# Performance work log

Hardware: AMD Instinct MI355X
Metric: run time of the kernel (lower is better)

Reference implementation:

```python
import jax, jax.numpy as jnp
import numpy as np

K = 1024
H = 16
HID = 4 * K
EPS = 1e-5


def _layernorm(x, g, b):
    mu = jnp.mean(x, axis=-1, keepdims=True)
    var = jnp.var(x, axis=-1, keepdims=True)
    return (x - mu) * jax.lax.rsqrt(var + EPS) * g + b


def _attention(xq, xkv, wq, wk, wv, wo, bo, causal):
    b, t, e = xq.shape
    tc = xkv.shape[1]
    h, s = H, e // H
    scale = e ** (-0.25)  # applied to both q and k, as in the original
    q = (xq @ wq).reshape(b, t, h, s) * scale
    k = (xkv @ wk).reshape(b, tc, h, s) * scale
    v = (xkv @ wv).reshape(b, tc, h, s)
    dot = jnp.einsum('bqhs,bkhs->bhqk', q, k)  # (b,h,t,tc)
    if causal:
        mask = jnp.tril(jnp.ones((t, tc), dtype=bool))
        dot = jnp.where(mask, dot, jnp.finfo(dot.dtype).min)
    att = jax.nn.softmax(dot, axis=-1)
    out = jnp.einsum('bhqk,bkhs->bqhs', att, v).reshape(b, t, e)
    return out @ wo + bo


def setup_inputs() -> dict:
    key = jax.random.key(0)
    ks = jax.random.split(key, 16)
    sd = K ** -0.5
    inp = {
        'x': jax.random.normal(ks[0], (4, 1024, K), jnp.float32),
        'context': jax.random.normal(ks[1], (4, 1024, K), jnp.float32),
        'sa_wq': jax.random.normal(ks[2], (K, K), jnp.float32) * sd,
        'sa_wk': jax.random.normal(ks[3], (K, K), jnp.float32) * sd,
        'sa_wv': jax.random.normal(ks[4], (K, K), jnp.float32) * sd,
        'sa_wo': jax.random.normal(ks[5], (K, K), jnp.float32) * sd,
        'sa_bo': jnp.zeros((K,), jnp.float32),
        'ca_wq': jax.random.normal(ks[6], (K, K), jnp.float32) * sd,
        'ca_wk': jax.random.normal(ks[7], (K, K), jnp.float32) * sd,
        'ca_wv': jax.random.normal(ks[8], (K, K), jnp.float32) * sd,
        'ca_wo': jax.random.normal(ks[9], (K, K), jnp.float32) * sd,
        'ca_bo': jnp.zeros((K,), jnp.float32),
        'n1_g': jnp.ones((K,), jnp.float32), 'n1_b': jnp.zeros((K,), jnp.float32),
        'n2_g': jnp.ones((K,), jnp.float32), 'n2_b': jnp.zeros((K,), jnp.float32),
        'n3_g': jnp.ones((K,), jnp.float32), 'n3_b': jnp.zeros((K,), jnp.float32),
        'ff_w1': jax.random.normal(ks[10], (K, HID), jnp.float32) * sd,
        'ff_b1': jnp.zeros((HID,), jnp.float32),
        'ff_w2': jax.random.normal(ks[11], (HID, K), jnp.float32) * (HID ** -0.5),
        'ff_b2': jnp.zeros((K,), jnp.float32),
    }
    return inp


def reference(x, context, sa_wq, sa_wk, sa_wv, sa_wo, sa_bo,
              ca_wq, ca_wk, ca_wv, ca_wo, ca_bo,
              n1_g, n1_b, n2_g, n2_b, n3_g, n3_b,
              ff_w1, ff_b1, ff_w2, ff_b2):
    # Masked self-attention + residual + LN (dropout is identity in eval mode)
    sa = _attention(x, x, sa_wq, sa_wk, sa_wv, sa_wo, sa_bo, causal=True)
    x = _layernorm(x + sa, n1_g, n1_b)
    # Cross-attention + residual + LN
    ca = _attention(x, context, ca_wq, ca_wk, ca_wv, ca_wo, ca_bo, causal=False)
    x = _layernorm(x + ca, n2_g, n2_b)
    # FFN + residual + LN
    ff = jax.nn.relu(x @ ff_w1 + ff_b1) @ ff_w2 + ff_b2
    x = _layernorm(x + ff, n3_g, n3_b)
    return x
```

## Files before the change

kernel.cpp:

```cpp
#include <hip/hip_runtime.h>

typedef __bf16 bf16x8 __attribute__((ext_vector_type(8)));
typedef __bf16 bf16x4 __attribute__((ext_vector_type(4)));
typedef float floatx4 __attribute__((ext_vector_type(4)));

#define EMB 1024
#define MROWS 4096
#define HIDN 4096
#define PSTRIDE ((size_t)MROWS * EMB)

__device__ __forceinline__ void load_lds16(const __bf16* g, __bf16* l) {
    __builtin_amdgcn_global_load_lds(
        (const __attribute__((address_space(1))) void*)g,
        (__attribute__((address_space(3))) void*)l, 16, 0, 0);
}

struct TJobs { const float* s[16]; __bf16* d[16]; int sld[16]; int dld[16]; };
__global__ void transpose_cast16_kernel(TJobs a) {
    __shared__ float tile[32][33];
    int jz = blockIdx.z;
    const float* in = a.s[jz];
    __bf16* out = a.d[jz];
    int sld = a.sld[jz], dld = a.dld[jz];
    int tx = threadIdx.x, ty = threadIdx.y;
    int c0 = blockIdx.x * 32, r0 = blockIdx.y * 32;
#pragma unroll
    for (int i = 0; i < 32; i += 8)
        tile[ty + i][tx] = in[(size_t)(r0 + ty + i) * sld + c0 + tx];
    __syncthreads();
#pragma unroll
    for (int i = 0; i < 32; i += 8)
        out[(size_t)(c0 + ty + i) * dld + r0 + tx] = (__bf16)tile[tx][ty + i];
}

__global__ void transpose_v_kernel(const __bf16* __restrict__ in,
                                   __bf16* __restrict__ vt, int ld, int Tc) {
    __shared__ __bf16 tile[32][33];
    int tx = threadIdx.x, ty = threadIdx.y;
    int t0 = blockIdx.x * 32, s0 = blockIdx.y * 32;
    int bh = blockIdx.z, b = bh >> 4, h = bh & 15;
#pragma unroll
    for (int i = 0; i < 32; i += 8)
        tile[ty + i][tx] = in[(size_t)(b * Tc + t0 + ty + i) * ld + h * 64 + s0 + tx];
    __syncthreads();
#pragma unroll
    for (int i = 0; i < 32; i += 8)
        vt[((size_t)bh * 64 + s0 + ty + i) * Tc + t0 + tx] = tile[tx][ty + i];
}

__global__ void cast_bf16_kernel(const float* __restrict__ in,
                                 __bf16* __restrict__ out, int n) {
    int i = (blockIdx.x * 256 + threadIdx.x) * 4;
    if (i >= n) return;
    float4 v = *(const float4*)(in + i);
    bf16x4 o;
    o[0] = (__bf16)v.x; o[1] = (__bf16)v.y; o[2] = (__bf16)v.z; o[3] = (__bf16)v.w;
    *(bf16x4*)(out + i) = o;
}

template <int RELU, int REG>
__launch_bounds__(256, 4)
__global__ void gemm_bt(const __bf16* __restrict__ A, const __bf16* __restrict__ A2,
                        int asplit, const __bf16* __restrict__ Bt,
                        __bf16* __restrict__ cb, __bf16* __restrict__ cbalt,
                        const float* __restrict__ bias,
                        int M, int N, int Kd, float scale0, float scale1,
                        int split, int fx, int fy) {
    __shared__ alignas(16) __bf16 smem[2 * 128 * 32];
    __bf16* As = smem;
    __bf16* Bs = smem + 128 * 32;
    int tid  = threadIdx.x;
    int wv   = tid >> 6, lane = tid & 63;

    int L   = blockIdx.x + gridDim.x * (blockIdx.y + gridDim.y * blockIdx.z);
    int xcd = L & 7, j = L >> 3;
    int ff  = fx * fy;
    int zw  = xcd / ff;
    int rr  = xcd % ff;
    int nxf = gridDim.x / fx;
    int bnw = (j % nxf) * fx + (rr % fx);
    int bmw = (j / nxf) * fy + (rr / fx);
    int bn  = bnw * 128, bm = bmw * 128;

    int wm   = (wv & 1) * 64, wn = (wv >> 1) * 64;
    int l16  = lane & 15, g16 = lane >> 4;

    int kc   = Kd / gridDim.z;
    int zoff = zw * kc;

    const __bf16* Ause = (bn >= asplit) ? A2 : A;

    const __bf16* ag0 = Ause + (size_t)(bm + (tid >> 2)) * Kd + zoff + (tid & 3) * 8;
    const __bf16* ag1 = ag0 + (size_t)64 * Kd;
    const __bf16* bg0 = Bt + (size_t)(bn + (tid >> 2)) * Kd + zoff + (tid & 3) * 8;
    const __bf16* bg1 = bg0 + (size_t)64 * Kd;
    __bf16* al0 = &As[tid * 8];
    __bf16* al1 = &As[2048 + tid * 8];
    __bf16* bl0 = &Bs[tid * 8];
    __bf16* bl1 = &Bs[2048 + tid * 8];

    floatx4 acc[4][4] = {};

    if (REG) {
        bf16x8 pa0 = *(const bf16x8*)ag0;
        bf16x8 pa1 = *(const bf16x8*)ag1;
        bf16x8 pb0 = *(const bf16x8*)bg0;
        bf16x8 pb1 = *(const bf16x8*)bg1;
        for (int k0 = 0; k0 < kc; k0 += 32) {
            *(bf16x8*)al0 = pa0;
            *(bf16x8*)al1 = pa1;
            *(bf16x8*)bl0 = pb0;
            *(bf16x8*)bl1 = pb1;
            if (k0 + 32 < kc) {
                ag0 += 32; ag1 += 32; bg0 += 32; bg1 += 32;
                pa0 = *(const bf16x8*)ag0;
                pa1 = *(const bf16x8*)ag1;
                pb0 = *(const bf16x8*)bg0;
                pb1 = *(const bf16x8*)bg1;
            }
            __syncthreads();
            bf16x8 af[4], bfr[4];
#pragma unroll
            for (int i = 0; i < 4; ++i)
                af[i] = *(const bf16x8*)&As[(wm + i * 16 + l16) * 32 + g16 * 8];
#pragma unroll
            for (int jj = 0; jj < 4; ++jj)
                bfr[jj] = *(const bf16x8*)&Bs[(wn + jj * 16 + l16) * 32 + g16 * 8];
#pragma unroll
            for (int i = 0; i < 4; ++i)
#pragma unroll
                for (int jj = 0; jj < 4; ++jj)
                    acc[i][jj] = __builtin_amdgcn_mfma_f32_16x16x32_bf16(af[i], bfr[jj], acc[i][jj], 0, 0, 0);
            __syncthreads();
        }
    } else {
        for (int k0 = 0; k0 < kc; k0 += 32) {
            __syncthreads();
            load_lds16(ag0, al0); load_lds16(ag1, al1);
            load_lds16(bg0, bl0); load_lds16(bg1, bl1);
            ag0 += 32; ag1 += 32; bg0 += 32; bg1 += 32;
            __syncthreads();
            bf16x8 af[4], bfr[4];
#pragma unroll
            for (int i = 0; i < 4; ++i)
                af[i] = *(const bf16x8*)&As[(wm + i * 16 + l16) * 32 + g16 * 8];
#pragma unroll
            for (int jj = 0; jj < 4; ++jj)
                bfr[jj] = *(const bf16x8*)&Bs[(wn + jj * 16 + l16) * 32 + g16 * 8];
#pragma unroll
            for (int i = 0; i < 4; ++i)
#pragma unroll
                for (int jj = 0; jj < 4; ++jj)
                    acc[i][jj] = __builtin_amdgcn_mfma_f32_16x16x32_bf16(af[i], bfr[jj], acc[i][jj], 0, 0, 0);
        }
        __syncthreads();
    }

    __bf16* Cp = (zw == 0) ? cb : cbalt + (size_t)(zw - 1) * M * N;
    const float* bz = (zw == 0) ? bias : nullptr;

    __bf16* eb = smem + wv * 2048;
    int erow = lane >> 2;
    int ecol = (lane & 3) * 16;
#pragma unroll
    for (int i = 0; i < 4; ++i) {
#pragma unroll
        for (int jj = 0; jj < 4; ++jj) {
            int col  = bn + wn + jj * 16 + l16;
            float sc = (col < split) ? scale0 : scale1;
            float bv = bz ? bz[col] : 0.f;
#pragma unroll
            for (int r = 0; r < 4; ++r) {
                float v = acc[i][jj][r] * sc + bv;
                if (RELU) v = fmaxf(v, 0.f);
                eb[(g16 * 4 + r) * 76 + jj * 16 + l16] = (__bf16)v;
            }
        }
        bf16x8 t0 = *(const bf16x8*)&eb[erow * 76 + ecol];
        bf16x8 t1 = *(const bf16x8*)&eb[erow * 76 + ecol + 8];
        size_t gb = (size_t)(bm + wm + i * 16 + erow) * N + bn + wn + ecol;
        *(bf16x8*)&Cp[gb]     = t0;
        *(bf16x8*)&Cp[gb + 8] = t1;
    }
}


#define VM4 asm volatile("s_waitcnt vmcnt(4)" ::: "memory")
#define VM0 asm volatile("s_waitcnt vmcnt(0)" ::: "memory")

#define STG(GB, HROWS, LDST, TILE)                                             \
    do {                                                                       \
        load_lds16((GB) + (size_t)(HROWS) * Kd + (TILE) * 64, (LDST) + tid8);  \
        load_lds16((GB) + (size_t)((HROWS) + 128) * Kd + (TILE) * 64,          \
                   (LDST) + 4096 + tid8);                                      \
    } while (0)

#define RD_A(ABUF, QM)                                                         \
    _Pragma("unroll")                                                          \
    for (int i2 = 0; i2 < 4; ++i2) {                                           \
        int s_ = (QM) * 128 + wr64 + i2 * 16 + l16;                            \
        a_[i2][0] = *(const bf16x8*)&(ABUF)[s_ * 64 + pa0];                    \
        a_[i2][1] = *(const bf16x8*)&(ABUF)[s_ * 64 + pa1];                    \
    }

#define RD_B(BBUF, QN, BREG)                                                   \
    _Pragma("unroll")                                                          \
    for (int j2 = 0; j2 < 2; ++j2) {                                           \
        int s_ = (QN) * 128 + wc32 + j2 * 16 + l16;                            \
        BREG[j2][0] = *(const bf16x8*)&(BBUF)[s_ * 64 + pa0];                  \
        BREG[j2][1] = *(const bf16x8*)&(BBUF)[s_ * 64 + pa1];                  \
    }

#define CORE(QM, QN, BREG, STAGE, TAIL)                                         \
    {                                                                           \
        STAGE;                                                                  \
        __builtin_amdgcn_s_setprio(1);                                          \
        _Pragma("unroll")                                                       \
        for (int i2 = 0; i2 < 4; ++i2)                                          \
            _Pragma("unroll")                                                   \
            for (int j2 = 0; j2 < 2; ++j2) {                                    \
                acc[(QM) * 4 + i2][(QN) * 2 + j2] =                             \
                    __builtin_amdgcn_mfma_f32_16x16x32_bf16(                    \
                        a_[i2][0], BREG[j2][0],                                 \
                        acc[(QM) * 4 + i2][(QN) * 2 + j2], 0, 0, 0);            \
                acc[(QM) * 4 + i2][(QN) * 2 + j2] =                             \
                    __builtin_amdgcn_mfma_f32_16x16x32_bf16(                    \
                        a_[i2][1], BREG[j2][1],                                 \
                        acc[(QM) * 4 + i2][(QN) * 2 + j2], 0, 0, 0);            \
            }                                                                   \
        __builtin_amdgcn_s_setprio(0);                                          \
        TAIL;                                                                   \
        __builtin_amdgcn_s_barrier();                                           \
    }

template <int RELU>
__launch_bounds__(512, 2)
__global__ void gemm256(const __bf16* __restrict__ A, const __bf16* __restrict__ A2,
                        int asplit, const __bf16* __restrict__ Bt,
                        __bf16* __restrict__ C, __bf16* __restrict__ Calt,
                        const float* __restrict__ bias,
                        int M, int N, int Kd, float scale0, float scale1,
                        int split, int pw) {
    __shared__ alignas(16) __bf16 smem[65536];
    __bf16* Alds0 = smem;
    __bf16* Alds1 = smem + 16384;
    __bf16* Blds0 = smem + 32768;
    __bf16* Blds1 = smem + 49152;

    int tid = threadIdx.x;
    int wv = tid >> 6, lane = tid & 63;
    int l16 = lane & 15, g16 = lane >> 4;
    int wr = wv >> 2, wc = wv & 3;
    int wr64 = wr * 64, wc32 = wc * 32;
    int pa0 = (g16 ^ (l16 & 7)) * 8;
    int pa1 = pa0 ^ 32;

    int L = blockIdx.x;
    int xcd = L & 7, jj = L >> 3;
    int bm = ((xcd >> 1) * 4 + jj / pw) * 256;
    int bn = ((xcd & 1) * pw + jj % pw) * 256;

    int z = blockIdx.y;
    int kc = Kd / gridDim.y;
    int zoff = z * kc;

    const __bf16* Ause = (bn >= asplit) ? A2 : A;
    int tid8 = tid * 8;
    int colOff = ((tid & 7) ^ ((tid >> 3) & 7)) * 8;
    const __bf16* baseA = Ause + (size_t)(bm + (tid >> 3)) * Kd + zoff + colOff;
    const __bf16* baseB = Bt + (size_t)(bn + (tid >> 8) * 64 + ((tid >> 3) & 31)) * Kd + zoff + colOff;

    floatx4 acc[8][4] = {};
    bf16x8 a_[4][2], b0_[2][2], b1_[2][2];

    STG(baseA, 0,  Alds0,        0);
    STG(baseB, 0,  Blds0,        0);
    STG(baseA, 64, Alds0 + 8192, 0);
    STG(baseB, 32, Blds0 + 8192, 0);
    STG(baseA, 0,  Alds1,        1);
    STG(baseB, 0,  Blds1,        1);
    VM4;
    __builtin_amdgcn_s_barrier();

    int niter = kc >> 7;
    for (int t = 0; t < niter - 1; ++t) {
        int tv = 2 * t + 1, tn0 = 2 * t + 2, tn1 = 2 * t + 3;
        RD_B(Blds0, 0, b0_); RD_A(Alds0, 0);
        CORE(0, 0, b0_, STG(baseA, 64, Alds1 + 8192, tv),  (void)0);
        RD_B(Blds0, 1, b1_);
        CORE(0, 1, b1_, STG(baseB, 32, Blds1 + 8192, tv),  (void)0);
        RD_A(Alds0, 1);
        CORE(1, 0, b0_, STG(baseA, 0,  Alds0,        tn0), (void)0);
        CORE(1, 1, b1_, STG(baseB, 0,  Blds0,        tn0), VM4);
        RD_B(Blds1, 0, b0_); RD_A(Alds1, 0);
        CORE(0, 0, b0_, STG(baseA, 64, Alds0 + 8192, tn0), (void)0);
        RD_B(Blds1, 1, b1_);
        CORE(0, 1, b1_, STG(baseB, 32, Blds0 + 8192, tn0), (void)0);
        RD_A(Alds1, 1);
        CORE(1, 0, b0_, STG(baseA, 0,  Alds1,        tn1), (void)0);
        CORE(1, 1, b1_, STG(baseB, 0,  Blds1,        tn1), VM4);
    }
    {
        int tv = (kc >> 6) - 1;
        RD_B(Blds0, 0, b0_); RD_A(Alds0, 0);
        CORE(0, 0, b0_, STG(baseA, 64, Alds1 + 8192, tv), (void)0);
        RD_B(Blds0, 1, b1_);
        CORE(0, 1, b1_, STG(baseB, 32, Blds1 + 8192, tv), (void)0);
        RD_A(Alds0, 1);
        CORE(1, 0, b0_, (void)0, (void)0);
        CORE(1, 1, b1_, (void)0, VM0);
        RD_B(Blds1, 0, b0_); RD_A(Alds1, 0);
        CORE(0, 0, b0_, (void)0, (void)0);
        RD_B(Blds1, 1, b1_);
        CORE(0, 1, b1_, (void)0, (void)0);
        RD_A(Alds1, 1);
        CORE(1, 0, b0_, (void)0, (void)0);
        CORE(1, 1, b1_, (void)0, (void)0);
    }

    __syncthreads();

    __bf16* Cp = (z == 0) ? C : Calt + (size_t)(z - 1) * M * N;
    const float* bz = (z == 0) ? bias : nullptr;

    __bf16* eb = smem + wv * 1216;
    int erow = lane >> 2;
    int ecol = (lane & 3) * 16;
    float sc[4], bv[4];
#pragma unroll
    for (int j = 0; j < 4; ++j) {
        int col = bn + wc * 64 + j * 16 + l16;
        sc[j] = (col < split) ? scale0 : scale1;
        bv[j] = bz ? bz[col] : 0.f;
    }
#pragma unroll
    for (int i = 0; i < 8; ++i) {
#pragma unroll
        for (int j = 0; j < 4; ++j) {
#pragma unroll
            for (int r = 0; r < 4; ++r) {
                float v = acc[i][j][r] * sc[j] + bv[j];
                if (RELU) v = fmaxf(v, 0.f);
                eb[(g16 * 4 + r) * 76 + j * 16 + l16] = (__bf16)v;
            }
        }
        bf16x8 t0 = *(const bf16x8*)&eb[erow * 76 + ecol];
        bf16x8 t1 = *(const bf16x8*)&eb[erow * 76 + ecol + 8];
        size_t gb = (size_t)(bm + wr * 128 + i * 16 + erow) * N + bn + wc * 64 + ecol;
        *(bf16x8*)&Cp[gb]     = t0;
        *(bf16x8*)&Cp[gb + 8] = t1;
    }
}

__launch_bounds__(256, 3)
__global__ void attn_kernel(const __bf16* __restrict__ qb, const __bf16* __restrict__ kb,
                            const __bf16* __restrict__ vt, int ldq, int ldk,
                            __bf16* __restrict__ out, int causal, int Tc) {
    constexpr int T = 1024;
    __shared__ alignas(16) __bf16 Qs[128 * 72];
    __shared__ alignas(16) __bf16 Ks[64 * 72];
    __shared__ alignas(16) __bf16 Vs[64 * 72];
    __shared__ alignas(16) __bf16 Ps[4][16 * 72];

    int tid = threadIdx.x;
    int wv = tid >> 6, lane = tid & 63;
    int l16 = lane & 15, g16 = lane >> 4;

    int L = blockIdx.x;
    int xcd = L & 7, idx = L >> 3;
    int i3 = idx & 7;
    int qt2 = (idx & 32) ? (7 - i3) : i3;
    int pair = xcd + 8 * (idx >> 3);
    int h = pair & 15, b = pair >> 4;

    int r0 = tid >> 3, s8 = (tid & 7) * 8;
    int r1 = r0 + 32;

#pragma unroll
    for (int p = 0; p < 4; ++p) {
        int row = r0 + p * 32;
        bf16x8 qv = *(const bf16x8*)(qb + (size_t)(b * T + qt2 * 128 + row) * ldq + h * 64 + s8);
        *(bf16x8*)&Qs[row * 72 + s8] = qv;
    }

    floatx4 oacc[2][4] = {};
    float li[2] = {0.f, 0.f};

    int ktend = causal ? (2 * qt2 + 2) : (Tc / 64);

    const __bf16* kbase = kb + (size_t)b * Tc * ldk + h * 64 + s8;
    const __bf16* vbase = vt + (size_t)(b * 16 + h) * 64 * Tc + s8;

    bf16x8 kc0 = *(const bf16x8*)(kbase + (size_t)r0 * ldk);
    bf16x8 kc1 = *(const bf16x8*)(kbase + (size_t)r1 * ldk);
    bf16x8 vc0 = *(const bf16x8*)(vbase + (size_t)r0 * Tc);
    bf16x8 vc1 = *(const bf16x8*)(vbase + (size_t)r1 * Tc);
    bf16x8 kn0, kn1, vn0, vn1;

    for (int kt = 0; kt < ktend; ++kt) {
        __syncthreads();
        *(bf16x8*)&Ks[r0 * 72 + s8] = kc0;
        *(bf16x8*)&Ks[r1 * 72 + s8] = kc1;
        *(bf16x8*)&Vs[r0 * 72 + s8] = vc0;
        *(bf16x8*)&Vs[r1 * 72 + s8] = vc1;
        if (kt + 1 < ktend) {
            const __bf16* kp = kbase + (size_t)(kt + 1) * 64 * ldk;
            const __bf16* vp = vbase + (size_t)(kt + 1) * 64;
            kn0 = *(const bf16x8*)(kp + (size_t)r0 * ldk);
            kn1 = *(const bf16x8*)(kp + (size_t)r1 * ldk);
            vn0 = *(const bf16x8*)(vp + (size_t)r0 * Tc);
            vn1 = *(const bf16x8*)(vp + (size_t)r1 * Tc);
        }
        __syncthreads();

#pragma unroll
        for (int sub = 0; sub < 2; ++sub) {
            if (causal && kt > 2 * qt2 + sub) continue;

            floatx4 sacc[4] = {};
#pragma unroll
            for (int kk = 0; kk < 2; ++kk) {
                bf16x8 bq = *(const bf16x8*)&Qs[(sub * 64 + wv * 16 + l16) * 72 + kk * 32 + g16 * 8];
#pragma unroll
                for (int j = 0; j < 4; ++j) {
                    bf16x8 ak = *(const bf16x8*)&Ks[(j * 16 + l16) * 72 + kk * 32 + g16 * 8];
                    sacc[j] = __builtin_amdgcn_mfma_f32_16x16x32_bf16(ak, bq, sacc[j], 0, 0, 0);
                }
            }
            if (causal && kt == 2 * qt2 + sub) {
                int qloc = wv * 16 + l16;
#pragma unroll
                for (int j = 0; j < 4; ++j)
#pragma unroll
                    for (int r = 0; r < 4; ++r)
                        if (j * 16 + g16 * 4 + r > qloc) sacc[j][r] = -1e30f;
            }

#pragma unroll
            for (int j = 0; j < 4; ++j) {
                bf16x4 pk;
#pragma unroll
                for (int r = 0; r < 4; ++r) {
                    float p = __builtin_amdgcn_exp2f(sacc[j][r]);
                    li[sub] += p;
                    pk[r] = (__bf16)p;
                }
                *(bf16x4*)&Ps[wv][l16 * 72 + j * 16 + g16 * 4] = pk;
            }
#pragma unroll
            for (int kk = 0; kk < 2; ++kk) {
                bf16x8 bp = *(const bf16x8*)&Ps[wv][l16 * 72 + kk * 32 + g16 * 8];
#pragma unroll
                for (int j = 0; j < 4; ++j) {
                    bf16x8 av = *(const bf16x8*)&Vs[(j * 16 + l16) * 72 + kk * 32 + g16 * 8];
                    oacc[sub][j] = __builtin_amdgcn_mfma_f32_16x16x32_bf16(av, bp, oacc[sub][j], 0, 0, 0);
                }
            }
        }
        kc0 = kn0; kc1 = kn1; vc0 = vn0; vc1 = vn1;
    }

    li[0] += __shfl_xor(li[0], 16); li[0] += __shfl_xor(li[0], 32);
    li[1] += __shfl_xor(li[1], 16); li[1] += __shfl_xor(li[1], 32);

    __syncthreads();
    int rw = lane >> 2, c4 = (lane & 3) * 16;
#pragma unroll
    for (int sub = 0; sub < 2; ++sub) {
        float inv = 1.f / li[sub];
#pragma unroll
        for (int j = 0; j < 4; ++j) {
            bf16x4 ok;
#pragma unroll
            for (int r = 0; r < 4; ++r) ok[r] = (__bf16)(oacc[sub][j][r] * inv);
            *(bf16x4*)&Ks[(wv * 16 + l16) * 72 + j * 16 + g16 * 4] = ok;
        }
        bf16x8 o0 = *(const bf16x8*)&Ks[(wv * 16 + rw) * 72 + c4];
        bf16x8 o1 = *(const bf16x8*)&Ks[(wv * 16 + rw) * 72 + c4 + 8];
        size_t ob = (size_t)(b * T + qt2 * 128 + sub * 64 + wv * 16 + rw) * EMB + h * 64 + c4;
        *(bf16x8*)&out[ob]     = o0;
        *(bf16x8*)&out[ob + 8] = o1;
    }
}

__launch_bounds__(256)
__global__ void ln_kernel(const float* __restrict__ res,
                          const __bf16* __restrict__ pb, int np,
                          const float* __restrict__ g, const float* __restrict__ be,
                          float* __restrict__ outf, __bf16* __restrict__ outb) {
    __shared__ float red[8];
    int row = blockIdx.x, tid = threadIdx.x;
    size_t base = (size_t)row * EMB;
    float4 v = ((const float4*)(res + base))[tid];
    for (int i = 0; i < np; ++i) {
        bf16x4 u = *(const bf16x4*)(pb + i * PSTRIDE + base + tid * 4);
        v.x += (float)u[0]; v.y += (float)u[1];
        v.z += (float)u[2]; v.w += (float)u[3];
    }
    float s  = v.x + v.y + v.z + v.w;
    float ss = v.x * v.x + v.y * v.y + v.z * v.z + v.w * v.w;
#pragma unroll
    for (int o = 1; o < 64; o <<= 1) { s += __shfl_xor(s, o); ss += __shfl_xor(ss, o); }
    if ((tid & 63) == 0) { red[(tid >> 6) * 2] = s; red[(tid >> 6) * 2 + 1] = ss; }
    __syncthreads();
    s  = red[0] + red[2] + red[4] + red[6];
    ss = red[1] + red[3] + red[5] + red[7];
    float mu  = s * (1.0f / 1024.0f);
    float var = ss * (1.0f / 1024.0f) - mu * mu;
    float rs  = rsqrtf(var + 1e-5f);
    float4 gg = ((const float4*)g)[tid];
    float4 bb = ((const float4*)be)[tid];
    float4 y;
    y.x = (v.x - mu) * rs * gg.x + bb.x;
    y.y = (v.y - mu) * rs * gg.y + bb.y;
    y.z = (v.z - mu) * rs * gg.z + bb.z;
    y.w = (v.w - mu) * rs * gg.w + bb.w;
    ((float4*)(outf + base))[tid] = y;
    if (outb) {
        bf16x4 o;
        o[0] = (__bf16)y.x; o[1] = (__bf16)y.y; o[2] = (__bf16)y.z; o[3] = (__bf16)y.w;
        *(bf16x4*)(outb + base + tid * 4) = o;
    }
}

extern "C" void kernel_launch(void* const* d_in, const int* in_sizes, int n_in,
                              void* d_out, int out_size, void* d_ws, size_t ws_size,
                              hipStream_t stream) {
    const float* x     = (const float*)d_in[0];
    const float* ctx   = (const float*)d_in[1];
    const float* sa_wq = (const float*)d_in[2];
    const float* sa_wk = (const float*)d_in[3];
    const float* sa_wv = (const float*)d_in[4];
    const float* sa_wo = (const float*)d_in[5];
    const float* sa_bo = (const float*)d_in[6];
    const float* ca_wq = (const float*)d_in[7];
    const float* ca_wk = (const float*)d_in[8];
    const float* ca_wv = (const float*)d_in[9];
    const float* ca_wo = (const float*)d_in[10];
    const float* ca_bo = (const float*)d_in[11];
    const float* n1_g = (const float*)d_in[12];
    const float* n1_b = (const float*)d_in[13];
    const float* n2_g = (const float*)d_in[14];
    const float* n2_b = (const float*)d_in[15];
    const float* n3_g = (const float*)d_in[16];
    const float* n3_b = (const float*)d_in[17];
    const float* ff_w1 = (const float*)d_in[18];
    const float* ff_b1 = (const float*)d_in[19];
    const float* ff_w2 = (const float*)d_in[20];
    const float* ff_b2 = (const float*)d_in[21];

    size_t off = 0;
    auto alloc = [&](size_t bytes) {
        void* p = (char*)d_ws + off;
        off += (bytes + 255) & ~(size_t)255;
        return p;
    };
    __bf16* w_sa_qkvT = (__bf16*)alloc((size_t)3 * EMB * EMB * 2);
    __bf16* w_sa_oT   = (__bf16*)alloc((size_t)EMB * EMB * 2);
    __bf16* w_ca_kvqT = (__bf16*)alloc((size_t)3 * EMB * EMB * 2);
    __bf16* w_ca_oT   = (__bf16*)alloc((size_t)EMB * EMB * 2);
    __bf16* w1T       = (__bf16*)alloc((size_t)HIDN * EMB * 2);
    __bf16* w2T       = (__bf16*)alloc((size_t)EMB * HIDN * 2);
    __bf16* xb        = (__bf16*)alloc((size_t)MROWS * EMB * 2);
    __bf16* qkv       = (__bf16*)alloc((size_t)MROWS * 3 * EMB * 2);
    __bf16* ao        = (__bf16*)alloc((size_t)MROWS * EMB * 2);
    __bf16* hid       = (__bf16*)alloc((size_t)MROWS * HIDN * 2);
    __bf16* x1b       = (__bf16*)alloc((size_t)MROWS * EMB * 2);
    __bf16* vt        = (__bf16*)alloc((size_t)MROWS * EMB * 2);
    float* res1       = (float*)alloc((size_t)MROWS * EMB * 4);
    float* res2       = (float*)alloc((size_t)MROWS * EMB * 4);

    __bf16* qkvc = qkv;
    __bf16* pbo  = qkv;
    __bf16* pbf  = xb;

    const float QSC = 0.04508422002778011f;
    const int   BIG = 1 << 30;
    dim3 tb(32, 8);

    TJobs tj;
    tj.s[0] = sa_wq; tj.d[0] = w_sa_qkvT;                          tj.sld[0] = EMB;  tj.dld[0] = EMB;
    tj.s[1] = sa_wk; tj.d[1] = w_sa_qkvT + (size_t)EMB * EMB;      tj.sld[1] = EMB;  tj.dld[1] = EMB;
    tj.s[2] = sa_wv; tj.d[2] = w_sa_qkvT + (size_t)2 * EMB * EMB;  tj.sld[2] = EMB;  tj.dld[2] = EMB;
    tj.s[3] = sa_wo; tj.d[3] = w_sa_oT;                            tj.sld[3] = EMB;  tj.dld[3] = EMB;
    tj.s[4] = ca_wk; tj.d[4] = w_ca_kvqT;                          tj.sld[4] = EMB;  tj.dld[4] = EMB;
    tj.s[5] = ca_wv; tj.d[5] = w_ca_kvqT + (size_t)EMB * EMB;      tj.sld[5] = EMB;  tj.dld[5] = EMB;
    tj.s[6] = ca_wq; tj.d[6] = w_ca_kvqT + (size_t)2 * EMB * EMB;  tj.sld[6] = EMB;  tj.dld[6] = EMB;
    tj.s[7] = ca_wo; tj.d[7] = w_ca_oT;                            tj.sld[7] = EMB;  tj.dld[7] = EMB;
    for (int c = 0; c < 4; ++c) {
        tj.s[8 + c] = ff_w1 + (size_t)c * 1024;
        tj.d[8 + c] = w1T + (size_t)c * 1024 * 1024;
        tj.sld[8 + c] = HIDN; tj.dld[8 + c] = EMB;
    }
    for (int c = 0; c < 4; ++c) {
        tj.s[12 + c] = ff_w2 + (size_t)c * 1024 * 1024;
        tj.d[12 + c] = w2T + (size_t)c * 1024;
        tj.sld[12 + c] = EMB; tj.dld[12 + c] = HIDN;
    }
    transpose_cast16_kernel<<<dim3(32, 32, 16), tb, 0, stream>>>(tj);

    cast_bf16_kernel<<<4096, 256, 0, stream>>>(x, xb, MROWS * EMB);
    gemm256<0><<<192, 512, 0, stream>>>(xb, xb, BIG, w_sa_qkvT,
        qkv, nullptr, nullptr, MROWS, 3 * EMB, EMB, QSC, 1.f, 1024, 6);
    transpose_v_kernel<<<dim3(32, 2, 64), tb, 0, stream>>>(qkv + 2 * EMB, vt, 3 * EMB, 1024);
    attn_kernel<<<512, 256, 0, stream>>>(qkv, qkv + EMB, vt, 3 * EMB, 3 * EMB, ao, 1, 1024);
    gemm_bt<0, 1><<<dim3(8, 32, 2), 256, 0, stream>>>(ao, ao, BIG, w_sa_oT,
        pbo, pbo + PSTRIDE, sa_bo, MROWS, EMB, EMB, 1.f, 1.f, 0, 2, 2);
    ln_kernel<<<4096, 256, 0, stream>>>(x, pbo, 2, n1_g, n1_b, res1, x1b);

    cast_bf16_kernel<<<4096, 256, 0, stream>>>(ctx, xb, MROWS * EMB);
    gemm256<0><<<192, 512, 0, stream>>>(xb, x1b, 2048, w_ca_kvqT,
        qkvc, nullptr, nullptr, MROWS, 3 * EMB, EMB, 1.f, QSC, 2048, 6);
    transpose_v_kernel<<<dim3(32, 2, 64), tb, 0, stream>>>(qkvc + EMB, vt, 3 * EMB, 1024);
    attn_kernel<<<512, 256, 0, stream>>>(qkvc + 2 * EMB, qkvc, vt, 3 * EMB, 3 * EMB, ao, 0, 1024);
    gemm_bt<0, 1><<<dim3(8, 32, 2), 256, 0, stream>>>(ao, ao, BIG, w_ca_oT,
        pbo, pbo + PSTRIDE, ca_bo, MROWS, EMB, EMB, 1.f, 1.f, 0, 2, 2);
    ln_kernel<<<4096, 256, 0, stream>>>(res1, pbo, 2, n2_g, n2_b, res2, x1b);

    gemm256<1><<<256, 512, 0, stream>>>(x1b, x1b, BIG, w1T,
        hid, nullptr, ff_b1, MROWS, HIDN, EMB, 1.f, 1.f, 0, 8);
    gemm256<0><<<dim3(64, 4), 512, 0, stream>>>(hid, hid, BIG, w2T,
        pbf, pbf + PSTRIDE, ff_b2, MROWS, EMB, HIDN, 1.f, 1.f, 0, 2);
    ln_kernel<<<4096, 256, 0, stream>>>(res2, pbf, 4, n3_g, n3_b, (float*)d_out, nullptr);
}
```

Before: 438.1 us.

## Use 256-tile split-K GEMM for output projections and batch input casts

Both attention output projections move from the 128x128 gemm_bt kernel (2-way split-K) to the gemm256 kernel with 4-way split-K, writing partials into the hidden buffer, and the layernorm now reduces 4 partials. The x and context fp32-to-bf16 casts are merged into one launch, with the context copy stored in the res2 buffer before res2 is written later. This is meant to raise MFMA efficiency on the output projections and cut one launch, at the cost of more partial-sum traffic in the layernorm.

```diff
diff --git a/kernel.cpp b/kernel.cpp
--- a/kernel.cpp
+++ b/kernel.cpp
@@ -48,140 +48,18 @@
         vt[((size_t)bh * 64 + s0 + ty + i) * Tc + t0 + tx] = tile[tx][ty + i];
 }
 
-__global__ void cast_bf16_kernel(const float* __restrict__ in,
-                                 __bf16* __restrict__ out, int n) {
+__global__ void cast2_bf16_kernel(const float* __restrict__ a,
+                                  const float* __restrict__ b,
+                                  __bf16* __restrict__ oa,
+                                  __bf16* __restrict__ ob, int n) {
     int i = (blockIdx.x * 256 + threadIdx.x) * 4;
-    if (i >= n) return;
+    const float* in = a;
+    __bf16* out = oa;
+    if (i >= n) { i -= n; in = b; out = ob; }
     float4 v = *(const float4*)(in + i);
     bf16x4 o;
     o[0] = (__bf16)v.x; o[1] = (__bf16)v.y; o[2] = (__bf16)v.z; o[3] = (__bf16)v.w;
     *(bf16x4*)(out + i) = o;
-}
-
-template <int RELU, int REG>
-__launch_bounds__(256, 4)
-__global__ void gemm_bt(const __bf16* __restrict__ A, const __bf16* __restrict__ A2,
-                        int asplit, const __bf16* __restrict__ Bt,
-                        __bf16* __restrict__ cb, __bf16* __restrict__ cbalt,
-                        const float* __restrict__ bias,
-                        int M, int N, int Kd, float scale0, float scale1,
-                        int split, int fx, int fy) {
-    __shared__ alignas(16) __bf16 smem[2 * 128 * 32];
-    __bf16* As = smem;
-    __bf16* Bs = smem + 128 * 32;
-    int tid  = threadIdx.x;
-    int wv   = tid >> 6, lane = tid & 63;
-
-    int L   = blockIdx.x + gridDim.x * (blockIdx.y + gridDim.y * blockIdx.z);
-    int xcd = L & 7, j = L >> 3;
-    int ff  = fx * fy;
-    int zw  = xcd / ff;
-    int rr  = xcd % ff;
-    int nxf = gridDim.x / fx;
-    int bnw = (j % nxf) * fx + (rr % fx);
-    int bmw = (j / nxf) * fy + (rr / fx);
-    int bn  = bnw * 128, bm = bmw * 128;
-
-    int wm   = (wv & 1) * 64, wn = (wv >> 1) * 64;
-    int l16  = lane & 15, g16 = lane >> 4;
-
-    int kc   = Kd / gridDim.z;
-    int zoff = zw * kc;
-
-    const __bf16* Ause = (bn >= asplit) ? A2 : A;
-
-    const __bf16* ag0 = Ause + (size_t)(bm + (tid >> 2)) * Kd + zoff + (tid & 3) * 8;
-    const __bf16* ag1 = ag0 + (size_t)64 * Kd;
-    const __bf16* bg0 = Bt + (size_t)(bn + (tid >> 2)) * Kd + zoff + (tid & 3) * 8;
-    const __bf16* bg1 = bg0 + (size_t)64 * Kd;
-    __bf16* al0 = &As[tid * 8];
-    __bf16* al1 = &As[2048 + tid * 8];
-    __bf16* bl0 = &Bs[tid * 8];
-    __bf16* bl1 = &Bs[2048 + tid * 8];
-
-    floatx4 acc[4][4] = {};
-
-    if (REG) {
-        bf16x8 pa0 = *(const bf16x8*)ag0;
-        bf16x8 pa1 = *(const bf16x8*)ag1;
-        bf16x8 pb0 = *(const bf16x8*)bg0;
-        bf16x8 pb1 = *(const bf16x8*)bg1;
-        for (int k0 = 0; k0 < kc; k0 += 32) {
-            *(bf16x8*)al0 = pa0;
-            *(bf16x8*)al1 = pa1;
-            *(bf16x8*)bl0 = pb0;
-            *(bf16x8*)bl1 = pb1;
-            if (k0 + 32 < kc) {
-                ag0 += 32; ag1 += 32; bg0 += 32; bg1 += 32;
-                pa0 = *(const bf16x8*)ag0;
-                pa1 = *(const bf16x8*)ag1;
-                pb0 = *(const bf16x8*)bg0;
-                pb1 = *(const bf16x8*)bg1;
-            }
-            __syncthreads();
-            bf16x8 af[4], bfr[4];
-#pragma unroll
-            for (int i = 0; i < 4; ++i)
-                af[i] = *(const bf16x8*)&As[(wm + i * 16 + l16) * 32 + g16 * 8];
-#pragma unroll
-            for (int jj = 0; jj < 4; ++jj)
-                bfr[jj] = *(const bf16x8*)&Bs[(wn + jj * 16 + l16) * 32 + g16 * 8];
-#pragma unroll
-            for (int i = 0; i < 4; ++i)
-#pragma unroll
-                for (int jj = 0; jj < 4; ++jj)
-                    acc[i][jj] = __builtin_amdgcn_mfma_f32_16x16x32_bf16(af[i], bfr[jj], acc[i][jj], 0, 0, 0);
-            __syncthreads();
-        }
-    } else {
-        for (int k0 = 0; k0 < kc; k0 += 32) {
-            __syncthreads();
-            load_lds16(ag0, al0); load_lds16(ag1, al1);
-            load_lds16(bg0, bl0); load_lds16(bg1, bl1);
-            ag0 += 32; ag1 += 32; bg0 += 32; bg1 += 32;
-            __syncthreads();
-            bf16x8 af[4], bfr[4];
-#pragma unroll
-            for (int i = 0; i < 4; ++i)
-                af[i] = *(const bf16x8*)&As[(wm + i * 16 + l16) * 32 + g16 * 8];
-#pragma unroll
-            for (int jj = 0; jj < 4; ++jj)
-                bfr[jj] = *(const bf16x8*)&Bs[(wn + jj * 16 + l16) * 32 + g16 * 8];
-#pragma unroll
-            for (int i = 0; i < 4; ++i)
-#pragma unroll
-                for (int jj = 0; jj < 4; ++jj)
-                    acc[i][jj] = __builtin_amdgcn_mfma_f32_16x16x32_bf16(af[i], bfr[jj], acc[i][jj], 0, 0, 0);
-        }
-        __syncthreads();
-    }
-
-    __bf16* Cp = (zw == 0) ? cb : cbalt + (size_t)(zw - 1) * M * N;
-    const float* bz = (zw == 0) ? bias : nullptr;
-
-    __bf16* eb = smem + wv * 2048;
-    int erow = lane >> 2;
-    int ecol = (lane & 3) * 16;
-#pragma unroll
-    for (int i = 0; i < 4; ++i) {
-#pragma unroll
-        for (int jj = 0; jj < 4; ++jj) {
-            int col  = bn + wn + jj * 16 + l16;
-            float sc = (col < split) ? scale0 : scale1;
-            float bv = bz ? bz[col] : 0.f;
-#pragma unroll
-            for (int r = 0; r < 4; ++r) {
-                float v = acc[i][jj][r] * sc + bv;
-                if (RELU) v = fmaxf(v, 0.f);
-                eb[(g16 * 4 + r) * 76 + jj * 16 + l16] = (__bf16)v;
-            }
-        }
-        bf16x8 t0 = *(const bf16x8*)&eb[erow * 76 + ecol];
-        bf16x8 t1 = *(const bf16x8*)&eb[erow * 76 + ecol + 8];
-        size_t gb = (size_t)(bm + wm + i * 16 + erow) * N + bn + wn + ecol;
-        *(bf16x8*)&Cp[gb]     = t0;
-        *(bf16x8*)&Cp[gb + 8] = t1;
-    }
 }
 
 
@@ -571,8 +449,8 @@
     float* res2       = (float*)alloc((size_t)MROWS * EMB * 4);
 
     __bf16* qkvc = qkv;
-    __bf16* pbo  = qkv;
     __bf16* pbf  = xb;
+    __bf16* ctxb = (__bf16*)res2;
 
     const float QSC = 0.04508422002778011f;
     const int   BIG = 1 << 30;
@@ -599,23 +477,23 @@
     }
     transpose_cast16_kernel<<<dim3(32, 32, 16), tb, 0, stream>>>(tj);
 
-    cast_bf16_kernel<<<4096, 256, 0, stream>>>(x, xb, MROWS * EMB);
+    cast2_bf16_kernel<<<8192, 256, 0, stream>>>(x, ctx, xb, ctxb, MROWS * EMB);
+
     gemm256<0><<<192, 512, 0, stream>>>(xb, xb, BIG, w_sa_qkvT,
         qkv, nullptr, nullptr, MROWS, 3 * EMB, EMB, QSC, 1.f, 1024, 6);
     transpose_v_kernel<<<dim3(32, 2, 64), tb, 0, stream>>>(qkv + 2 * EMB, vt, 3 * EMB, 1024);
     attn_kernel<<<512, 256, 0, stream>>>(qkv, qkv + EMB, vt, 3 * EMB, 3 * EMB, ao, 1, 1024);
-    gemm_bt<0, 1><<<dim3(8, 32, 2), 256, 0, stream>>>(ao, ao, BIG, w_sa_oT,
-        pbo, pbo + PSTRIDE, sa_bo, MROWS, EMB, EMB, 1.f, 1.f, 0, 2, 2);
-    ln_kernel<<<4096, 256, 0, stream>>>(x, pbo, 2, n1_g, n1_b, res1, x1b);
-
-    cast_bf16_kernel<<<4096, 256, 0, stream>>>(ctx, xb, MROWS * EMB);
-    gemm256<0><<<192, 512, 0, stream>>>(xb, x1b, 2048, w_ca_kvqT,
+    gemm256<0><<<dim3(64, 4), 512, 0, stream>>>(ao, ao, BIG, w_sa_oT,
+        hid, hid + PSTRIDE, sa_bo, MROWS, EMB, EMB, 1.f, 1.f, 0, 2);
+    ln_kernel<<<4096, 256, 0, stream>>>(x, hid, 4, n1_g, n1_b, res1, x1b);
+
+    gemm256<0><<<192, 512, 0, stream>>>(ctxb, x1b, 2048, w_ca_kvqT,
         qkvc, nullptr, nullptr, MROWS, 3 * EMB, EMB, 1.f, QSC, 2048, 6);
     transpose_v_kernel<<<dim3(32, 2, 64), tb, 0, stream>>>(qkvc + EMB, vt, 3 * EMB, 1024);
     attn_kernel<<<512, 256, 0, stream>>>(qkvc + 2 * EMB, qkvc, vt, 3 * EMB, 3 * EMB, ao, 0, 1024);
-    gemm_bt<0, 1><<<dim3(8, 32, 2), 256, 0, stream>>>(ao, ao, BIG, w_ca_oT,
-        pbo, pbo + PSTRIDE, ca_bo, MROWS, EMB, EMB, 1.f, 1.f, 0, 2, 2);
-    ln_kernel<<<4096, 256, 0, stream>>>(res1, pbo, 2, n2_g, n2_b, res2, x1b);
+    gemm256<0><<<dim3(64, 4), 512, 0, stream>>>(ao, ao, BIG, w_ca_oT,
+        hid, hid + PSTRIDE, ca_bo, MROWS, EMB, EMB, 1.f, 1.f, 0, 2);
+    ln_kernel<<<4096, 256, 0, stream>>>(res1, hid, 4, n2_g, n2_b, res2, x1b);
 
     gemm256<1><<<256, 512, 0, stream>>>(x1b, x1b, BIG, w1T,
         hid, nullptr, ff_b1, MROWS, HIDN, EMB, 1.f, 1.f, 0, 8);
```

Measured after the change: 445.7 us. Within noise of the previous version (+1.7%).
